# Kernel tuning notes

Measured on AMD Instinct MI355X. Metric: run time of the kernel, lower is better.

The kernel has to match this reference:

```python
import jax, jax.numpy as jnp
import numpy as np

B, L, PRED = 32, 1024, 256
CIN = 32            # enc_in == dec_in == c_out
DM, DFF, H, M = 512, 2048, 8, 64
E = DM // H
EL, DL = 2, 1
K = 25              # moving-avg kernel


def moving_avg(x):
    # torch: replicate-pad (K-1)//2 on both ends, then AvgPool1d(K, stride=1)
    pad = (K - 1) // 2
    xp = jnp.concatenate([jnp.repeat(x[:, :1], pad, axis=1), x, jnp.repeat(x[:, -1:], pad, axis=1)], axis=1)
    cs = jnp.cumsum(xp, axis=1)
    cs = jnp.concatenate([jnp.zeros_like(cs[:, :1]), cs], axis=1)
    return (cs[:, K:] - cs[:, :-K]) / K


def decomp(x):
    ma = moving_avg(x)
    return x - ma, ma


def circ_conv3(x, W):
    # Conv1d(kernel=3, padding=1, padding_mode='circular', bias=False); x:[B,L,C], W:[O,C,3]
    xp = jnp.concatenate([x[:, -1:], x, x[:, :1]], axis=1)
    win = jnp.stack([xp[:, :-2], xp[:, 1:-1], xp[:, 2:]], axis=-1)  # [B,L,C,3]
    return jnp.einsum('blcj,ocj->blo', win, W)


def pos_emb():
    pos = jnp.arange(L, dtype=jnp.float32)[:, None]
    div = jnp.exp(jnp.arange(0, DM, 2, dtype=jnp.float32) * (-np.log(10000.0) / DM))
    pe = jnp.zeros((L, DM), dtype=jnp.float32)
    pe = pe.at[:, 0::2].set(jnp.sin(pos * div))
    pe = pe.at[:, 1::2].set(jnp.cos(pos * div))
    return pe


def fourier_self(q, k, v, w):
    # FourierBlock: rFFT over time, keep lowest M modes, per-(head,mode) complex matmul, irFFT
    Bq, Lq = q.shape[0], q.shape[1]
    xft = jnp.fft.rfft(q.transpose(0, 2, 3, 1), axis=-1)[..., :M]        # [B,H,E,M]
    wc = w[..., 0] + 1j * w[..., 1]                                      # [H,E,E,M]
    om = jnp.einsum('bhem,heom->bhom', xft, wc)
    out_ft = jnp.zeros((Bq, H, E, Lq // 2 + 1), dtype=om.dtype).at[..., :M].set(om)
    return jnp.fft.irfft(out_ft, n=Lq, axis=-1).transpose(0, 3, 1, 2)    # [B,L,H,E]


def fourier_cross(q, k, v, w):
    # FourierCrossAttention (activation='tanh'); note official code uses k-modes as values
    Bq, Lq = q.shape[0], q.shape[1]
    xq = jnp.fft.rfft(q.transpose(0, 2, 3, 1), axis=-1)[..., :M]         # [B,H,E,M]
    xk = jnp.fft.rfft(k.transpose(0, 2, 3, 1), axis=-1)[..., :M]
    qk = jnp.tanh(jnp.einsum('bhex,bhey->bhxy', xq, xk))                 # complex tanh
    qkv = jnp.einsum('bhxy,bhey->bhex', qk, xk)
    wc = w[..., 0] + 1j * w[..., 1]
    om = jnp.einsum('bhex,heox->bhox', qkv, wc)
    out_ft = jnp.zeros((Bq, H, E, Lq // 2 + 1), dtype=om.dtype).at[..., :M].set(om)
    return jnp.fft.irfft(out_ft / (DM * DM), n=Lq, axis=-1).transpose(0, 3, 1, 2)


def mha(xq, xkv, Wq, bq, Wk, bk, Wv, bv, Wo, bo, inner, fw):
    Bq, Lq = xq.shape[0], xq.shape[1]
    q = (xq @ Wq.T + bq).reshape(Bq, Lq, H, E)
    k = (xkv @ Wk.T + bk).reshape(Bq, -1, H, E)
    v = (xkv @ Wv.T + bv).reshape(Bq, -1, H, E)
    o = inner(q, k, v, fw).reshape(Bq, Lq, DM)
    return o @ Wo.T + bo


def setup_inputs():
    ks = iter(jax.random.split(jax.random.key(0), 80))
    p = lambda shape: jax.random.normal(next(ks), shape, dtype=jnp.float32) * 0.02
    z = lambda shape: jnp.zeros(shape, dtype=jnp.float32)
    d = {}
    d['x_enc'] = jax.random.normal(next(ks), (B, L, CIN), dtype=jnp.float32)
    d['tok_W'] = p((DM, CIN, 3))
    for pre, n in (('enc_', EL), ('dec_s', DL), ('dec_c', DL)):
        for nm in ('Wq', 'Wk', 'Wv', 'Wo'):
            d[pre + nm] = p((n, DM, DM))
        for nm in ('bq', 'bk', 'bv', 'bo'):
            d[pre + nm] = z((n, DM))
    d['enc_c1W'] = p((EL, DFF, DM)); d['enc_c1b'] = z((EL, DFF))
    d['enc_c2W'] = p((EL, DM, DFF)); d['enc_c2b'] = z((EL, DM))
    d['dec_c1W'] = p((DL, DFF, DM)); d['dec_c1b'] = z((DL, DFF))
    d['dec_c2W'] = p((DL, DM, DFF)); d['dec_c2b'] = z((DL, DM))
    d['dec_trW'] = p((DL, CIN, DM, 3))
    d['fb_enc'] = p((H, E, E, M, 2))
    d['fb_dec'] = p((H, E, E, M, 2))
    d['fc_w'] = p((H, E, E, M, 2))
    d['p1W'] = p((CIN, CIN)); d['p1b'] = z((CIN,))
    d['p2W'] = p((PRED, L)); d['p2b'] = z((PRED,))
    d['p3W'] = p((CIN, DM)); d['p3b'] = z((CIN,))
    return d


def reference(x_enc, tok_W, enc_Wq, enc_Wk, enc_Wv, enc_Wo, enc_bq, enc_bk, enc_bv, enc_bo,
              dec_sWq, dec_sWk, dec_sWv, dec_sWo, dec_sbq, dec_sbk, dec_sbv, dec_sbo,
              dec_cWq, dec_cWk, dec_cWv, dec_cWo, dec_cbq, dec_cbk, dec_cbv, dec_cbo,
              enc_c1W, enc_c1b, enc_c2W, enc_c2b, dec_c1W, dec_c1b, dec_c2W, dec_c2b,
              dec_trW, fb_enc, fb_dec, fc_w, p1W, p1b, p2W, p2b, p3W, p3b):
    seasonal_init, trend_init = decomp(x_enc)
    enc = circ_conv3(x_enc, tok_W) + pos_emb()[None]   # DataEmbedding (eval: no dropout)
    for l in range(EL):
        h = enc + mha(enc, enc, enc_Wq[l], enc_bq[l], enc_Wk[l], enc_bk[l], enc_Wv[l], enc_bv[l],
                      enc_Wo[l], enc_bo[l], fourier_self, fb_enc)
        h, _ = decomp(h)
        y = jax.nn.relu(h @ enc_c1W[l].T + enc_c1b[l]) @ enc_c2W[l].T + enc_c2b[l]
        enc, _ = decomp(h + y)
    # NB: top-level source calls decoder(enc_out, enc_out, ...): dec_embedding output is unused
    x = enc
    trend = trend_init
    for l in range(DL):
        x = x + mha(x, x, dec_sWq[l], dec_sbq[l], dec_sWk[l], dec_sbk[l], dec_sWv[l], dec_sbv[l],
                    dec_sWo[l], dec_sbo[l], fourier_self, fb_dec)
        x, t1 = decomp(x)
        x = x + mha(x, enc, dec_cWq[l], dec_cbq[l], dec_cWk[l], dec_cbk[l], dec_cWv[l], dec_cbv[l],
                    dec_cWo[l], dec_cbo[l], fourier_cross, fc_w)
        x, t2 = decomp(x)
        y = jax.nn.relu(x @ dec_c1W[l].T + dec_c1b[l]) @ dec_c2W[l].T + dec_c2b[l]
        x, t3 = decomp(x + y)
        trend = trend + circ_conv3(t1 + t2 + t3, dec_trW[l])   # trend projection (circular conv3)
    out = trend + (x @ p3W.T + p3b)                            # [B,L,CIN]
    out = out @ p1W.T + p1b
    out = jnp.einsum('blc,pl->bpc', out, p2W) + p2b[None, :, None]  # proj2 over time -> [B,PRED,CIN]
    return out
```

## Files before the change

kernel.cpp:

```cpp
#include <hip/hip_runtime.h>
#include <math.h>

namespace {

constexpr int cB = 32, cL = 1024, cCIN = 32, cDM = 512, cDFF = 2048;
constexpr int cH = 8, cE = 64, cM = 64, cPRED = 256;
constexpr int M2 = 2 * cM;

typedef __attribute__((ext_vector_type(8))) short short8v;
typedef __attribute__((ext_vector_type(4))) float float4v;

__device__ inline unsigned short f2bf(float f) {
  unsigned int u = __builtin_bit_cast(unsigned int, f);
  u += 0x7FFFu + ((u >> 16) & 1u);
  return (unsigned short)(u >> 16);
}
__device__ inline float bf2f(unsigned short s) {
  return __builtin_bit_cast(float, (unsigned int)s << 16);
}

typedef const __attribute__((address_space(1))) unsigned int gu32_t;
typedef __attribute__((address_space(3))) unsigned int lu32_t;
__device__ inline void gld16(const void* g, void* l) {
  __builtin_amdgcn_global_load_lds((gu32_t*)g, (lu32_t*)l, 16, 0, 0);
}

__global__ void basis_kernel(short* __restrict__ basisdb, short* __restrict__ basisib) {
  int idx = blockIdx.x * 256 + threadIdx.x;
  if (idx >= M2 * cL) return;
  int t = idx & (cL - 1);
  int m2 = idx >> 10;
  int m = m2 >> 1;
  float ang = 6.2831853071795864f * (float)((m * t) & (cL - 1)) / (float)cL;
  float cv = cosf(ang), sv = sinf(ang);
  float vd = (m2 & 1) ? -sv : cv;
  basisdb[idx] = (short)f2bf(vd);
  float s = (m == 0) ? ((m2 & 1) ? 0.f : (1.f / (float)cL)) : (2.f / (float)cL);
  basisib[t * M2 + m2] = (short)f2bf(vd * s);
}

__global__ void pe_kernel(float* __restrict__ pe) {
  int idx = blockIdx.x * 256 + threadIdx.x;
  int o = idx & (cDM - 1), t = idx >> 9;
  int i = o >> 1;
  float freq = __expf((float)(2 * i) * (-9.210340371976184f / (float)cDM));
  float ang = freq * (float)t;
  pe[idx] = (o & 1) ? cosf(ang) : sinf(ang);
}

constexpr int NJOB = 14;
struct CvtArgs {
  const float* src[NJOB];
  short* dst[NJOB];
  int n[NJOB];
};
__global__ void cvtm_kernel(CvtArgs a) {
  int j = blockIdx.y;
  const float* s = a.src[j];
  short* d = a.dst[j];
  int n = a.n[j];
  for (int i = blockIdx.x * 256 + threadIdx.x; i < n; i += gridDim.x * 256)
    d[i] = (short)f2bf(s[i]);
}

__global__ void prep_kernel(const float* __restrict__ tok_W, const float* __restrict__ trW,
                            const float* __restrict__ p3W, const float* __restrict__ p3b,
                            short* __restrict__ Bpadb, short* __restrict__ Wtr3b,
                            short* __restrict__ p3padb, float* __restrict__ p3bpadf) {
  int idx = blockIdx.x * 256 + threadIdx.x;
  if (idx < 512 * 128) {
    int o = idx >> 7, s = idx & 127, j = s >> 5, c = s & 31;
    Bpadb[idx] = (j < 3) ? (short)f2bf(tok_W[o * 96 + c * 3 + j]) : (short)0;
  }
  if (idx < 128 * 1536) {
    int o = idx / 1536, r = idx % 1536, j = r >> 9, c = r & 511;
    Wtr3b[idx] = (o < 32) ? (short)f2bf(trW[(long)o * 1536 + c * 3 + j]) : (short)0;
  }
  if (idx < 128 * 512) {
    int o = idx >> 9, k = idx & 511;
    p3padb[idx] = (o < 32) ? (short)f2bf(p3W[o * 512 + k]) : (short)0;
  }
  if (idx < 128) p3bpadf[idx] = (idx < 32) ? p3b[idx] : 0.f;
}

__global__ void winbuild_kernel(const float* __restrict__ x, short* __restrict__ win) {
  int idx = blockIdx.x * 256 + threadIdx.x;
  int s4 = idx & 31;
  int row = idx >> 5;
  int t = row & (cL - 1), b = row >> 10;
  int j = s4 >> 3, c4 = s4 & 7;
  unsigned int lo = 0, hi = 0;
  if (j < 3) {
    int ts = (t + j + cL - 1) & (cL - 1);
    float4 v = *(const float4*)&x[((long)b * cL + ts) * cCIN + c4 * 4];
    lo = (unsigned int)f2bf(v.x) | ((unsigned int)f2bf(v.y) << 16);
    hi = (unsigned int)f2bf(v.z) | ((unsigned int)f2bf(v.w) << 16);
  }
  *(uint2*)&win[row * 128 + s4 * 4] = make_uint2(lo, hi);
}

__global__ __launch_bounds__(256) void transpose_bf(const short* __restrict__ in,
                                                    short* __restrict__ out) {
  __shared__ short tile[32][33];
  int b = blockIdx.z;
  in += (long)b * cL * cDM;
  out += (long)b * cL * cDM;
  int c0 = blockIdx.x * 32, t0 = blockIdx.y * 32;
  int tx = threadIdx.x & 31, ty = threadIdx.x >> 5;
#pragma unroll
  for (int r = 0; r < 32; r += 8) tile[ty + r][tx] = in[(long)(t0 + ty + r) * cDM + c0 + tx];
  __syncthreads();
#pragma unroll
  for (int r = 0; r < 32; r += 8)
    out[(long)(c0 + ty + r) * cL + t0 + tx] = tile[tx][ty + r];
}

__global__ void decomp_kernel(const float* __restrict__ x, float* __restrict__ maf, int n8,
                              int C) {
  int idx = blockIdx.x * 256 + threadIdx.x;
  if (idx >= n8) return;
  int c = idx % C;
  int u = idx / C;
  int t0 = (u & 127) * 8;
  int b = u >> 7;
  long base = (long)b * cL * C + c;
  float s = 0.f;
#pragma unroll
  for (int j = -12; j <= 12; j++) {
    int tt = t0 + j;
    tt = tt < 0 ? 0 : (tt >= cL ? cL - 1 : tt);
    s += x[base + (long)tt * C];
  }
#pragma unroll
  for (int k = 0; k < 8; k++) {
    int t = t0 + k;
    maf[base + (long)t * C] = s * (1.0f / 25.0f);
    int ta = t + 13;
    ta = ta >= cL ? cL - 1 : ta;
    int td = t - 12;
    td = td < 0 ? 0 : td;
    s += x[base + (long)ta * C] - x[base + (long)td * C];
  }
}

__global__ void decompb_kernel(const short* __restrict__ x, short* __restrict__ sb,
                               short* __restrict__ mab, int maacc, int n8, int C) {
  int idx = blockIdx.x * 256 + threadIdx.x;
  if (idx >= n8) return;
  int c = idx % C;
  int u = idx / C;
  int t0 = (u & 127) * 8;
  int b = u >> 7;
  long base = (long)b * cL * C + c;
  float s = 0.f;
#pragma unroll
  for (int j = -12; j <= 12; j++) {
    int tt = t0 + j;
    tt = tt < 0 ? 0 : (tt >= cL ? cL - 1 : tt);
    s += bf2f((unsigned short)x[base + (long)tt * C]);
  }
#pragma unroll
  for (int k = 0; k < 8; k++) {
    int t = t0 + k;
    long e = base + (long)t * C;
    float ma = s * (1.0f / 25.0f);
    if (sb) sb[e] = (short)f2bf(bf2f((unsigned short)x[e]) - ma);
    if (mab) {
      float v = maacc ? bf2f((unsigned short)mab[e]) + ma : ma;
      mab[e] = (short)f2bf(v);
    }
    int ta = t + 13;
    ta = ta >= cL ? cL - 1 : ta;
    int td = t - 12;
    td = td < 0 ? 0 : td;
    s += bf2f((unsigned short)x[base + (long)ta * C]) - bf2f((unsigned short)x[base + (long)td * C]);
  }
}

__global__ __launch_bounds__(256) void p2_kernel(const float* __restrict__ x,
                                                 const float* __restrict__ W,
                                                 const float* __restrict__ bias,
                                                 float* __restrict__ out) {
  __shared__ float tile[256 * 32];
  int b = blockIdx.x;
  int p0 = blockIdx.y * 8;
  int c = threadIdx.x & 31, pl = threadIdx.x >> 5;
  const float* xb = x + (long)b * cL * cCIN;
  const float* w = W + (long)(p0 + pl) * cL;
  float s = 0.f;
  for (int l0 = 0; l0 < cL; l0 += 256) {
    __syncthreads();
    for (int i = threadIdx.x; i < 256 * 32; i += 256) tile[i] = xb[(long)l0 * 32 + i];
    __syncthreads();
#pragma unroll 8
    for (int l = 0; l < 256; l++) s += tile[l * 32 + c] * w[l0 + l];
  }
  out[((long)b * cPRED + p0 + pl) * cCIN + c] = s + bias[p0 + pl];
}

__global__ __launch_bounds__(512) void modemix_t_kernel(const float* __restrict__ F,
                                                        const unsigned short* __restrict__ W,
                                                        short* __restrict__ Gt, float scale) {
  int b = blockIdx.x, h = blockIdx.y;
  __shared__ float2 Fs[cE][cM];
  __shared__ short ot[128][72];
  const float* Fb = F + ((long)b * cDM + h * cE) * M2;
  for (int i = threadIdx.x; i < cE * cM; i += 512) {
    int e = i >> 6, x = i & 63;
    Fs[e][x] = ((const float2*)(Fb + (long)e * M2))[x];
  }
  __syncthreads();
  int x = threadIdx.x & 63, og = threadIdx.x >> 6;
  float2 acc[8];
#pragma unroll
  for (int i = 0; i < 8; i++) acc[i] = make_float2(0.f, 0.f);
  for (int e = 0; e < cE; e++) {
    float2 f = Fs[e][x];
#pragma unroll
    for (int i = 0; i < 8; i++) {
      int o = og * 8 + i;
      unsigned int wu = *(const unsigned int*)&W[((((long)h * cE + e) * cE + o) * cM + x) * 2];
      float wx = bf2f((unsigned short)wu), wy = bf2f((unsigned short)(wu >> 16));
      acc[i].x += f.x * wx - f.y * wy;
      acc[i].y += f.x * wy + f.y * wx;
    }
  }
#pragma unroll
  for (int i = 0; i < 8; i++) {
    int o = og * 8 + i;
    ot[2 * x][o] = (short)f2bf(acc[i].x * scale);
    ot[2 * x + 1][o] = (short)f2bf(acc[i].y * scale);
  }
  __syncthreads();
  short* gb = Gt + (long)b * (M2 * cDM) + h * cE;
  for (int u = threadIdx.x; u < 1024; u += 512) {
    int row = u >> 3, seg = u & 7;
    *(uint4*)&gb[(long)row * cDM + seg * 8] = *(const uint4*)&ot[row][seg * 8];
  }
}

__global__ __launch_bounds__(1024) void fused_cross_kernel(const float* __restrict__ Fq,
                                                           const float* __restrict__ Fk,
                                                           const unsigned short* __restrict__ W,
                                                           short* __restrict__ Gt, float scale) {
  __shared__ __align__(16) char smem[65536];
  float2(*KsT)[cE] = (float2(*)[cE])smem;
  float2(*qks)[cM] = (float2(*)[cM])(smem + 32768);
  int b = blockIdx.x, h = blockIdx.y;
  const float* kb = Fk + ((long)b * cDM + h * cE) * M2;
  for (int i = threadIdx.x; i < cE * cM; i += 1024) {
    int e = i >> 6, y = i & 63;
    KsT[y][e] = ((const float2*)(kb + (long)e * M2))[y];
  }
  __syncthreads();
  {
    int x = threadIdx.x & 63, yg = threadIdx.x >> 6;
    const float* qb = Fq + ((long)b * cDM + h * cE) * M2;
    float2 acc[4];
#pragma unroll
    for (int i = 0; i < 4; i++) acc[i] = make_float2(0.f, 0.f);
    for (int e = 0; e < cE; e++) {
      float2 q = ((const float2*)(qb + (long)e * M2))[x];
#pragma unroll
      for (int i = 0; i < 4; i++) {
        float2 k = KsT[yg * 4 + i][e];
        acc[i].x += q.x * k.x - q.y * k.y;
        acc[i].y += q.x * k.y + q.y * k.x;
      }
    }
#pragma unroll
    for (int i = 0; i < 4; i++) {
      int y = yg * 4 + i;
      float a = acc[i].x, bi = acc[i].y;
      float re, im;
      float t2a = 2.f * a;
      if (fabsf(t2a) > 60.f) {
        re = t2a > 0.f ? 1.f : -1.f;
        im = 0.f;
      } else {
        float denom = coshf(t2a) + cosf(2.f * bi);
        re = sinhf(t2a) / denom;
        im = sinf(2.f * bi) / denom;
      }
      qks[y][x] = make_float2(re, im);
    }
  }
  __syncthreads();
  int e = threadIdx.x & 63, xg = threadIdx.x >> 6;
  float2 a2[4];
#pragma unroll
  for (int i = 0; i < 4; i++) a2[i] = make_float2(0.f, 0.f);
  for (int y = 0; y < cM; y++) {
    float2 k = KsT[y][e];
#pragma unroll
    for (int i = 0; i < 4; i++) {
      float2 qk = qks[y][xg * 4 + i];
      a2[i].x += qk.x * k.x - qk.y * k.y;
      a2[i].y += qk.x * k.y + qk.y * k.x;
    }
  }
  __syncthreads();
  float2(*Qv)[cM] = (float2(*)[cM])smem;
#pragma unroll
  for (int i = 0; i < 4; i++) Qv[e][xg * 4 + i] = a2[i];
  __syncthreads();
  {
    int x = threadIdx.x & 63, og = threadIdx.x >> 6;
    float2 m[4];
#pragma unroll
    for (int i = 0; i < 4; i++) m[i] = make_float2(0.f, 0.f);
    for (int ee = 0; ee < cE; ee++) {
      float2 f = Qv[ee][x];
#pragma unroll
      for (int i = 0; i < 4; i++) {
        int o = og * 4 + i;
        unsigned int wu = *(const unsigned int*)&W[((((long)h * cE + ee) * cE + o) * cM + x) * 2];
        float wx = bf2f((unsigned short)wu), wy = bf2f((unsigned short)(wu >> 16));
        m[i].x += f.x * wx - f.y * wy;
        m[i].y += f.x * wy + f.y * wx;
      }
    }
    short(*ot)[72] = (short(*)[72])(smem + 32768);
#pragma unroll
    for (int i = 0; i < 4; i++) {
      int o = og * 4 + i;
      ot[2 * x][o] = (short)f2bf(m[i].x * scale);
      ot[2 * x + 1][o] = (short)f2bf(m[i].y * scale);
    }
    __syncthreads();
    short* gb = Gt + (long)b * (M2 * cDM) + h * cE;
    int u = threadIdx.x;
    {
      int row = u >> 3, seg = u & 7;
      *(uint4*)&gb[(long)row * cDM + seg * 8] =
          *(const uint4*)&((short(*)[72])(smem + 32768))[row][seg * 8];
    }
  }
}

constexpr int GBM = 128, GBN = 128, GBK = 16, LPAD = 132;

__global__ __launch_bounds__(256) void gemm_kernel(const float* __restrict__ A,
                                                   const float* __restrict__ B,
                                                   const float* __restrict__ bias,
                                                   float* __restrict__ C, int M, int N, int K) {
  __shared__ float As[GBK][LPAD];
  __shared__ float Bs[GBK][LPAD];
  int n0 = blockIdx.x * GBN, m0 = blockIdx.y * GBM;
  int tid = threadIdx.x;
  int tx = tid & 15, ty = tid >> 4;
  float acc[8][8];
#pragma unroll
  for (int i = 0; i < 8; i++)
#pragma unroll
    for (int j = 0; j < 8; j++) acc[i][j] = 0.f;

  for (int k0 = 0; k0 < K; k0 += GBK) {
#pragma unroll
    for (int p = 0; p < 8; p++) {
      int i = p * 256 + tid;
      int mm = i >> 4, kk = i & 15;
      int gm = m0 + mm;
      As[kk][mm] = (gm < M && k0 + kk < K) ? A[(long)gm * K + k0 + kk] : 0.f;
    }
#pragma unroll
    for (int p = 0; p < 8; p++) {
      int i = p * 256 + tid;
      int nn = i >> 4, kk = i & 15;
      int gn = n0 + nn;
      Bs[kk][nn] = (gn < N && k0 + kk < K) ? B[(long)gn * K + k0 + kk] : 0.f;
    }
    __syncthreads();
#pragma unroll
    for (int kk = 0; kk < GBK; kk++) {
      float a[8], bb[8];
      *(float4*)&a[0] = *(const float4*)&As[kk][ty * 8];
      *(float4*)&a[4] = *(const float4*)&As[kk][ty * 8 + 4];
      *(float4*)&bb[0] = *(const float4*)&Bs[kk][tx * 8];
      *(float4*)&bb[4] = *(const float4*)&Bs[kk][tx * 8 + 4];
#pragma unroll
      for (int i = 0; i < 8; i++)
#pragma unroll
        for (int j = 0; j < 8; j++) acc[i][j] += a[i] * bb[j];
    }
    __syncthreads();
  }

  for (int i = 0; i < 8; i++) {
    int gm = m0 + ty * 8 + i;
    if (gm >= M) break;
    long rowoff = (long)gm * N;
    for (int j = 0; j < 8; j++) {
      int gn = n0 + tx * 8 + j;
      if (gn < N) C[rowoff + gn] = acc[i][j] + (bias ? bias[gn] : 0.f);
    }
  }
}

__global__ __launch_bounds__(512) void mfma_gemm256(
    const short* __restrict__ A, const short* __restrict__ B, const float* __restrict__ bias,
    const short* __restrict__ addendb, const float* __restrict__ pe, float* __restrict__ Cf,
    short* __restrict__ Cb, int M, int N, int K, int lda, int relu, int ldc) {
  __shared__ __align__(16) short As[16384];
  __shared__ __align__(16) short Bs[8192];
  int nwg = gridDim.x * gridDim.y;
  int orig = blockIdx.x + gridDim.x * blockIdx.y;
  int q = nwg >> 3, r = nwg & 7;
  int xcd = orig & 7, ii = orig >> 3;
  int flat = (xcd < r ? xcd * (q + 1) : r * (q + 1) + (xcd - r) * q) + ii;
  int bx = flat % (int)gridDim.x;
  int by = flat / (int)gridDim.x;

  int n0 = bx * 128, m0 = by * 256;
  int tid = threadIdx.x;
  int lane = tid & 63;
  int w = tid >> 6;
  int wm = w >> 1;
  int wn = w & 1;
  int lr = lane & 15, lg = lane >> 4;
  int lrow = lane >> 3;
  int scol = ((lane & 7) * 8) ^ (lrow << 3);

  float4v acc[4][4];
#pragma unroll
  for (int i = 0; i < 4; i++)
#pragma unroll
    for (int j = 0; j < 4; j++) acc[i][j] = (float4v){0.f, 0.f, 0.f, 0.f};

  int nk = K >> 6;
  int swr = (lr & 7) << 3;
  for (int t = 0; t < nk; ++t) {
    int k0 = t << 6;
#pragma unroll
    for (int j = 0; j < 4; j++) {
      int seg = w * 4 + j;
      int row = seg * 8 + lrow;
      gld16(A + (long)(m0 + row) * lda + k0 + scol, &As[seg * 512]);
    }
#pragma unroll
    for (int j = 0; j < 2; j++) {
      int seg = w * 2 + j;
      int row = seg * 8 + lrow;
      gld16(B + (long)(n0 + row) * K + k0 + scol, &Bs[seg * 512]);
    }
    asm volatile("s_waitcnt vmcnt(0)" ::: "memory");
    __syncthreads();
#pragma unroll
    for (int ks = 0; ks < 2; ks++) {
      short8v af[4], bfr[4];
#pragma unroll
      for (int mi = 0; mi < 4; mi++)
        af[mi] = *(const short8v*)&As[(wm * 64 + mi * 16 + lr) * 64 + ((ks * 32 + lg * 8) ^ swr)];
#pragma unroll
      for (int ni = 0; ni < 4; ni++)
        bfr[ni] = *(const short8v*)&Bs[(wn * 64 + ni * 16 + lr) * 64 + ((ks * 32 + lg * 8) ^ swr)];
#pragma unroll
      for (int mi = 0; mi < 4; mi++)
#pragma unroll
        for (int ni = 0; ni < 4; ni++)
          acc[mi][ni] =
              __builtin_amdgcn_mfma_f32_16x16x32_bf16(af[mi], bfr[ni], acc[mi][ni], 0, 0, 0);
    }
    __syncthreads();
  }

#pragma unroll
  for (int mi = 0; mi < 4; mi++) {
#pragma unroll
    for (int i = 0; i < 4; i++) {
      int gr = m0 + wm * 64 + mi * 16 + lg * 4 + i;
      long rowoff = (long)gr * ldc;
#pragma unroll
      for (int ni = 0; ni < 4; ni++) {
        int gc = n0 + wn * 64 + ni * 16 + lr;
        float v = acc[mi][ni][i];
        if (bias) v += bias[gc];
        if (pe) v += pe[((gr & (cL - 1)) << 9) + gc];
        if (addendb) v += bf2f((unsigned short)addendb[rowoff + gc]);
        if (relu) v = fmaxf(v, 0.f);
        if (Cf) Cf[rowoff + gc] = v;
        if (Cb) Cb[rowoff + gc] = (short)f2bf(v);
      }
    }
  }
}

__global__ __launch_bounds__(256) void mfma_gemm64(
    const short* __restrict__ A, const short* __restrict__ B, const float* __restrict__ bias,
    const float* __restrict__ addf, const short* __restrict__ addb,
    const float* __restrict__ m0b, float* __restrict__ Cf, short* __restrict__ Cb, int M, int N,
    int K, int lda, long sA, long sB, long sC, int Nreal, int ldc, int amode,
    const short* __restrict__ A2, const short* __restrict__ B2, const float* __restrict__ m0b2,
    float* __restrict__ Cf2, int zsplit) {
  __shared__ __align__(16) short As[4096];
  __shared__ __align__(16) short Bs[4096];
  int nwg = gridDim.x * gridDim.y * gridDim.z;
  int orig = blockIdx.x + gridDim.x * (blockIdx.y + gridDim.y * blockIdx.z);
  int q = nwg >> 3, r = nwg & 7;
  int xcd = orig & 7, ii = orig >> 3;
  int flat = (xcd < r ? xcd * (q + 1) : r * (q + 1) + (xcd - r) * q) + ii;
  int bx = flat % (int)gridDim.x;
  int tmp = flat / (int)gridDim.x;
  int by = tmp % (int)gridDim.y;
  int bz = tmp / (int)gridDim.y;

  int z = bz;
  if (zsplit > 0 && bz >= zsplit) {
    A = A2;
    B = B2;
    m0b = m0b2;
    Cf = Cf2;
    z = bz - zsplit;
  }
  A += (long)z * sA;
  B += (long)z * sB;
  if (Cf) Cf += (long)z * sC;
  if (Cb) Cb += (long)z * sC;
  const float* Ad = addf ? addf + (long)z * sC : nullptr;
  const short* Adb = addb ? addb + (long)z * sC : nullptr;
  int n0 = bx * 64, m0 = by * 64;
  int tid = threadIdx.x;
  int lane = tid & 63;
  int w = tid >> 6;
  int wm = w & 1, wn = w >> 1;
  int lr = lane & 15, lg = lane >> 4;
  int lrow = lane >> 3;
  int scol = ((lane & 7) * 8) ^ (lrow << 3);

  float4v acc[2][2];
#pragma unroll
  for (int i = 0; i < 2; i++)
#pragma unroll
    for (int j = 0; j < 2; j++) acc[i][j] = (float4v){0.f, 0.f, 0.f, 0.f};

  int nk = K >> 6;
  int swr = (lr & 7) << 3;
  for (int t = 0; t < nk; ++t) {
    int k0 = t << 6;
#pragma unroll
    for (int j = 0; j < 2; j++) {
      int seg = w * 2 + j;
      int row = seg * 8 + lrow;
      const short* ga;
      if (amode == 0) {
        ga = A + (long)(m0 + row) * lda + k0 + scol;
      } else {
        int r2 = m0 + row;
        int bb = r2 >> 10, tt = r2 & 1023;
        int jj = k0 >> 9, c0 = k0 & 511;
        ga = A + ((((long)(bb << 10)) | ((tt + jj + 1023) & 1023)) << 9) + c0 + scol;
      }
      gld16(ga, &As[seg * 512]);
      gld16(B + (long)(n0 + row) * K + k0 + scol, &Bs[seg * 512]);
    }
    asm volatile("s_waitcnt vmcnt(0)" ::: "memory");
    __syncthreads();
#pragma unroll
    for (int ks = 0; ks < 2; ks++) {
      short8v af[2], bfr[2];
#pragma unroll
      for (int mi = 0; mi < 2; mi++)
        af[mi] = *(const short8v*)&As[(wm * 32 + mi * 16 + lr) * 64 + ((ks * 32 + lg * 8) ^ swr)];
#pragma unroll
      for (int ni = 0; ni < 2; ni++)
        bfr[ni] = *(const short8v*)&Bs[(wn * 32 + ni * 16 + lr) * 64 + ((ks * 32 + lg * 8) ^ swr)];
#pragma unroll
      for (int mi = 0; mi < 2; mi++)
#pragma unroll
        for (int ni = 0; ni < 2; ni++)
          acc[mi][ni] =
              __builtin_amdgcn_mfma_f32_16x16x32_bf16(af[mi], bfr[ni], acc[mi][ni], 0, 0, 0);
    }
    __syncthreads();
  }

#pragma unroll
  for (int mi = 0; mi < 2; mi++) {
#pragma unroll
    for (int i = 0; i < 4; i++) {
      int gr = m0 + wm * 32 + mi * 16 + lg * 4 + i;
      long rowoff = (long)gr * ldc;
#pragma unroll
      for (int ni = 0; ni < 2; ni++) {
        int gc = n0 + wn * 32 + ni * 16 + lr;
        if (gc < Nreal) {
          float v = acc[mi][ni][i];
          if (bias) v += bias[gc];
          if (m0b && gc == 0) v += 1024.f * m0b[gr];
          if (Ad) v += Ad[rowoff + gc];
          if (Adb) v += bf2f((unsigned short)Adb[rowoff + gc]);
          if (Cf) Cf[rowoff + gc] = v;
          if (Cb) Cb[rowoff + gc] = (short)f2bf(v);
        }
      }
    }
  }
}

}

extern "C" void kernel_launch(void* const* d_in, const int* in_sizes, int n_in, void* d_out,
                              int out_size, void* d_ws, size_t ws_size, hipStream_t stream) {
  const float* x_enc = (const float*)d_in[0];
  const float* tok_W = (const float*)d_in[1];
  const float* enc_Wq = (const float*)d_in[2];
  const float* enc_Wo = (const float*)d_in[5];
  const float* enc_bq = (const float*)d_in[6];
  const float* enc_bo = (const float*)d_in[9];
  const float* dsWq = (const float*)d_in[10];
  const float* dsWo = (const float*)d_in[13];
  const float* dsbq = (const float*)d_in[14];
  const float* dsbo = (const float*)d_in[17];
  const float* dcWq = (const float*)d_in[18];
  const float* dcWk = (const float*)d_in[19];
  const float* dcWo = (const float*)d_in[21];
  const float* dcbq = (const float*)d_in[22];
  const float* dcbk = (const float*)d_in[23];
  const float* dcbo = (const float*)d_in[25];
  const float* enc_c1W = (const float*)d_in[26];
  const float* enc_c1b = (const float*)d_in[27];
  const float* enc_c2W = (const float*)d_in[28];
  const float* enc_c2b = (const float*)d_in[29];
  const float* dec_c1W = (const float*)d_in[30];
  const float* dec_c1b = (const float*)d_in[31];
  const float* dec_c2W = (const float*)d_in[32];
  const float* dec_c2b = (const float*)d_in[33];
  const float* dec_trW = (const float*)d_in[34];
  const float* fb_enc = (const float*)d_in[35];
  const float* fb_dec = (const float*)d_in[36];
  const float* fc_w = (const float*)d_in[37];
  const float* p1W = (const float*)d_in[38];
  const float* p1b = (const float*)d_in[39];
  const float* p2W = (const float*)d_in[40];
  const float* p2b = (const float*)d_in[41];
  const float* p3W = (const float*)d_in[42];
  const float* p3b = (const float*)d_in[43];

  constexpr long MIXW = 8L * 64 * 64 * 64 * 2;

  auto layout_bytes = [&](long BG, long RH) -> size_t {
    size_t t = 0;
    auto add = [&](size_t b) { t = (t + b + 255) & ~(size_t)255; };
    add(2 * 262144 * 2); add(2 * 262144 * 2);
    add(262144 * 2); add(262144 * 2); add(262144 * 2); add(262144 * 2); add(262144 * 2);
    add(2 * 1048576 * 2); add(2 * 1048576 * 2); add(1048576 * 2); add(1048576 * 2);
    add(131072 * 2); add(131072 * 2); add(65536 * 2); add(196608 * 2); add(65536 * 2);
    add(128 * 4); add(524288 * 4);
    add(MIXW * 2); add(MIXW * 2); add(MIXW * 2);
    long GA = BG * cL * cDM;
    add(GA * 2); add(GA * 2); add(GA * 2); add(GA * 2); add(GA * 2);
    add(BG * cL * 128 * 2);
    size_t ub = (size_t)GA * 2;
    size_t hd = (size_t)RH * cDFF * 2;
    add(ub > hd ? ub : hd);
    add(BG * 65536 * 4); add(BG * 65536 * 4);
    add(BG * 65536 * 2); add(BG * 65536 * 2); add(BG * 65536 * 2); add(BG * 65536 * 2);
    add(BG * cL * cCIN * 4); add(BG * cL * cCIN * 4); add(BG * cL * cCIN * 4);
    return t;
  };
  int BG = cB;
  while (BG > 1 && layout_bytes(BG, 512) > ws_size) BG >>= 1;
  long RH = (long)BG * cL;
  while (RH > 512 && layout_bytes(BG, RH) > ws_size) RH >>= 1;

  long GBL = (long)BG * cL;
  char* base = (char*)d_ws;
  size_t off = 0;
  auto alloc = [&](size_t bytes) -> void* {
    void* p = base + off;
    off = (off + bytes + 255) & ~(size_t)255;
    return p;
  };
  short* WqbE = (short*)alloc(2 * 262144 * 2);
  short* WobE = (short*)alloc(2 * 262144 * 2);
  short* dsWqb = (short*)alloc(262144 * 2);
  short* dsWob = (short*)alloc(262144 * 2);
  short* dcWqb = (short*)alloc(262144 * 2);
  short* dcWkb = (short*)alloc(262144 * 2);
  short* dcWob = (short*)alloc(262144 * 2);
  short* c1bE = (short*)alloc(2 * 1048576 * 2);
  short* c2bE = (short*)alloc(2 * 1048576 * 2);
  short* c1bD = (short*)alloc(1048576 * 2);
  short* c2bD = (short*)alloc(1048576 * 2);
  short* basisdb = (short*)alloc(131072 * 2);
  short* basisib = (short*)alloc(131072 * 2);
  short* Bpadb = (short*)alloc(65536 * 2);
  short* Wtr3b = (short*)alloc(196608 * 2);
  short* p3padb = (short*)alloc(65536 * 2);
  float* p3bpadf = (float*)alloc(128 * 4);
  float* pe = (float*)alloc(524288 * 4);
  short* fbEb = (short*)alloc(MIXW * 2);
  short* fbDb = (short*)alloc(MIXW * 2);
  short* fcwb = (short*)alloc(MIXW * 2);
  long GA = GBL * cDM;
  short* Eb = (short*)alloc(GA * 2);
  short* Xb = (short*)alloc(GA * 2);
  short* Ab = (short*)alloc(GA * 2);
  short* Sb = (short*)alloc(GA * 2);
  short* Yb = (short*)alloc(GA * 2);
  short* winb = (short*)alloc(GBL * 128 * 2);
  size_t ubsz = (size_t)GA * 2;
  size_t hdsz = (size_t)RH * cDFF * 2;
  short* UB = (short*)alloc(ubsz > hdsz ? ubsz : hdsz);
  short* Tb = UB;
  short* HDb = UB;
  float* Fq = (float*)alloc((size_t)BG * 65536 * 4);
  float* Fk = (float*)alloc((size_t)BG * 65536 * 4);
  short* FEb = (short*)alloc((size_t)BG * 65536 * 2);
  short* FXb = (short*)alloc((size_t)BG * 65536 * 2);
  short* Gtb = (short*)alloc((size_t)BG * 65536 * 2);
  short* Hb = (short*)alloc((size_t)BG * 65536 * 2);
  float* TRD = (float*)alloc(GBL * cCIN * 4);
  float* O1 = (float*)alloc(GBL * cCIN * 4);
  float* O2 = (float*)alloc(GBL * cCIN * 4);

  auto mg256 = [&](const short* Am, const short* Bm, const float* bias, const short* adb,
                   const float* peA, float* Cf, short* Cb, int Mm, int Nn, int Kk, int lda,
                   int relu, int ldc) {
    dim3 g(Nn / 128, Mm / 256);
    mfma_gemm256<<<g, 512, 0, stream>>>(Am, Bm, bias, adb, peA, Cf, Cb, Mm, Nn, Kk, lda, relu,
                                        ldc);
  };
  auto mg64 = [&](const short* Am, const short* Bm, const float* bias, const float* addf,
                  const short* addb, const float* m0b, float* Cf, short* Cb, int Mm, int Nn,
                  int Kk, int lda, long sA, long sB, long sC, int batch, int Nreal, int ldc,
                  int amode) {
    dim3 g(Nn / 64, Mm / 64, batch);
    mfma_gemm64<<<g, 256, 0, stream>>>(Am, Bm, bias, addf, addb, m0b, Cf, Cb, Mm, Nn, Kk, lda,
                                       sA, sB, sC, Nreal, ldc, amode, nullptr, nullptr, nullptr,
                                       nullptr, 0);
  };
  auto decompf = [&](const float* x, float* maf, long total, int C_) {
    int n8 = (int)(total / 8);
    decomp_kernel<<<(n8 + 255) / 256, 256, 0, stream>>>(x, maf, n8, C_);
  };
  auto decompb = [&](const short* x, short* sb, short* mab, int maacc, long total, int C_) {
    int n8 = (int)(total / 8);
    decompb_kernel<<<(n8 + 255) / 256, 256, 0, stream>>>(x, sb, mab, maacc, n8, C_);
  };
  auto dft = [&](const short* srcb, short* Fout) {
    transpose_bf<<<dim3(16, 32, BG), 256, 0, stream>>>(srcb, Tb);
    mg64(basisdb, Tb, nullptr, nullptr, nullptr, nullptr, nullptr, Fout, M2, cDM, cL, cL, 0,
         (long)cDM * cL, 65536, BG, cDM, cDM, 0);
  };
  auto modeproj = [&](const short* Wb, const short* Fin, const float* m0b, float* Cf, short* Cb) {
    mg64(Wb, Fin, nullptr, nullptr, nullptr, m0b, Cf, Cb, cDM, M2, cDM, cDM, 0, 65536, 65536, BG,
         M2, M2, 0);
  };
  auto modeproj2 = [&](const short* Wa, const short* Fa, const float* ba, float* Ca,
                       const short* Wb2, const short* Fb2, const float* bb2, float* Cb2) {
    dim3 g(M2 / 64, cDM / 64, 2 * BG);
    mfma_gemm64<<<g, 256, 0, stream>>>(Wa, Fa, nullptr, nullptr, nullptr, ba, Ca, nullptr, cDM,
                                       M2, cDM, cDM, 0, 65536, 65536, M2, M2, 0, Wb2, Fb2, bb2,
                                       Cb2, BG);
  };
  auto idft = [&](const short* Hin, const float* bias, const short* adb, short* Cbout) {
    mg64(basisib, Hin, bias, nullptr, adb, nullptr, nullptr, Cbout, cL, cDM, M2, M2, 0, 65536,
         (long)cL * cDM, BG, cDM, cDM, 0);
  };
  auto ffn = [&](const short* inb, const short* addb, short* outb, const short* c1w,
                 const float* c1bias, const short* c2w, const float* c2bias) {
    for (long r = 0; r < GBL; r += RH) {
      mg256(inb + r * cDM, c1w, c1bias, nullptr, nullptr, nullptr, HDb, (int)RH, cDFF, cDM, cDM,
            1, cDFF);
      mg256(HDb, c2w, c2bias, addb + r * cDM, nullptr, nullptr, outb + r * cDM, (int)RH, cDM,
            cDFF, cDFF, 0, cDM);
    }
  };
  auto trendg = [&](const short* mab) {
    mg64(mab, Wtr3b, nullptr, TRD, nullptr, nullptr, TRD, nullptr, (int)GBL, 64, 1536, 512, 0, 0,
         0, 1, cCIN, cCIN, 1);
  };
  auto mixt = [&](const float* F, const short* W, float scale) {
    modemix_t_kernel<<<dim3(BG, cH), 512, 0, stream>>>(F, (const unsigned short*)W, Gtb, scale);
  };

  basis_kernel<<<(M2 * cL) / 256, 256, 0, stream>>>(basisdb, basisib);
  pe_kernel<<<(cL * cDM) / 256, 256, 0, stream>>>(pe);
  prep_kernel<<<768, 256, 0, stream>>>(tok_W, dec_trW, p3W, p3b, Bpadb, Wtr3b, p3padb, p3bpadf);
  {
    CvtArgs ca;
    const float* srcs[NJOB] = {enc_Wq, enc_Wo, dsWq, dsWo, dcWq, dcWk, dcWo,
                               enc_c1W, enc_c2W, dec_c1W, dec_c2W, fb_enc, fb_dec, fc_w};
    short* dsts[NJOB] = {WqbE, WobE, dsWqb, dsWob, dcWqb, dcWkb, dcWob,
                         c1bE, c2bE, c1bD, c2bD, fbEb, fbDb, fcwb};
    int ns[NJOB] = {524288, 524288, 262144, 262144, 262144, 262144, 262144,
                    2097152, 2097152, 1048576, 1048576, (int)MIXW, (int)MIXW, (int)MIXW};
    for (int j = 0; j < NJOB; j++) {
      ca.src[j] = srcs[j];
      ca.dst[j] = dsts[j];
      ca.n[j] = ns[j];
    }
    cvtm_kernel<<<dim3(256, NJOB), 256, 0, stream>>>(ca);
  }

  for (int b0 = 0; b0 < cB; b0 += BG) {
    const float* xg = x_enc + (long)b0 * cL * cCIN;

    decompf(xg, TRD, GBL * cCIN, cCIN);
    winbuild_kernel<<<(int)(GBL * 32 / 256), 256, 0, stream>>>(xg, winb);
    mg256(winb, Bpadb, nullptr, nullptr, pe, nullptr, Eb, (int)GBL, cDM, 128, 128, 0, cDM);

    for (int l = 0; l < 2; l++) {
      dft(Eb, FEb);
      modeproj(WqbE + (long)l * 262144, FEb, enc_bq + l * cDM, Fq, nullptr);
      mixt(Fq, fbEb, 1.0f);
      modeproj(WobE + (long)l * 262144, Gtb, nullptr, nullptr, Hb);
      idft(Hb, enc_bo + l * cDM, Eb, Yb);
      decompb(Yb, Xb, nullptr, 0, GA, cDM);
      ffn(Xb, Xb, Yb, c1bE + (long)l * 1048576, enc_c1b + l * cDFF, c2bE + (long)l * 1048576,
          enc_c2b + l * cDM);
      decompb(Yb, Eb, nullptr, 0, GA, cDM);
    }

    dft(Eb, FEb);
    modeproj(dsWqb, FEb, dsbq, Fq, nullptr);
    mixt(Fq, fbDb, 1.0f);
    modeproj(dsWob, Gtb, nullptr, nullptr, Hb);
    idft(Hb, dsbo, Eb, Yb);
    decompb(Yb, Xb, Sb, 0, GA, cDM);
    dft(Xb, FXb);
    modeproj2(dcWqb, FXb, dcbq, Fq, dcWkb, FEb, dcbk, Fk);
    fused_cross_kernel<<<dim3(BG, cH), 1024, 0, stream>>>(Fq, Fk, (const unsigned short*)fcwb,
                                                          Gtb, 1.0f / (float)(cDM * cDM));
    modeproj(dcWob, Gtb, nullptr, nullptr, Hb);
    idft(Hb, dcbo, Xb, Yb);
    decompb(Yb, Ab, Sb, 1, GA, cDM);
    ffn(Ab, Ab, Yb, c1bD, dec_c1b, c2bD, dec_c2b);
    decompb(Yb, Xb, Sb, 1, GA, cDM);
    trendg(Sb);

    mg64(Xb, p3padb, p3bpadf, TRD, nullptr, nullptr, O1, nullptr, (int)GBL, 64, cDM, cDM, 0, 0,
         0, 1, cCIN, cCIN, 0);
    gemm_kernel<<<dim3(1, (int)(GBL / 128)), 256, 0, stream>>>(O1, p1W, p1b, O2, (int)GBL, cCIN,
                                                               cCIN);
    p2_kernel<<<dim3(BG, 32), 256, 0, stream>>>(O2, p2W, p2b,
                                                (float*)d_out + (long)b0 * cPRED * cCIN);
  }
}
```

Baseline: 2.101 ms.

## Fuse query mode projection with Fourier mode mixing; widen transpose tiles

```diff
diff --git a/kernel.cpp b/kernel.cpp
--- a/kernel.cpp
+++ b/kernel.cpp
@@ -101,17 +101,17 @@
 
 __global__ __launch_bounds__(256) void transpose_bf(const short* __restrict__ in,
                                                     short* __restrict__ out) {
-  __shared__ short tile[32][33];
+  __shared__ short tile[64][65];
   int b = blockIdx.z;
   in += (long)b * cL * cDM;
   out += (long)b * cL * cDM;
-  int c0 = blockIdx.x * 32, t0 = blockIdx.y * 32;
-  int tx = threadIdx.x & 31, ty = threadIdx.x >> 5;
-#pragma unroll
-  for (int r = 0; r < 32; r += 8) tile[ty + r][tx] = in[(long)(t0 + ty + r) * cDM + c0 + tx];
+  int c0 = blockIdx.x * 64, t0 = blockIdx.y * 64;
+  int tx = threadIdx.x & 63, ty = threadIdx.x >> 6;
+#pragma unroll
+  for (int r = 0; r < 64; r += 4) tile[ty + r][tx] = in[(long)(t0 + ty + r) * cDM + c0 + tx];
   __syncthreads();
 #pragma unroll
-  for (int r = 0; r < 32; r += 8)
+  for (int r = 0; r < 64; r += 4)
     out[(long)(c0 + ty + r) * cL + t0 + tx] = tile[tx][ty + r];
 }
 
@@ -198,42 +198,108 @@
   out[((long)b * cPRED + p0 + pl) * cCIN + c] = s + bias[p0 + pl];
 }
 
-__global__ __launch_bounds__(512) void modemix_t_kernel(const float* __restrict__ F,
-                                                        const unsigned short* __restrict__ W,
-                                                        short* __restrict__ Gt, float scale) {
+__global__ __launch_bounds__(256) void projmix_kernel(const short* __restrict__ W,
+                                                      const short* __restrict__ Fin,
+                                                      const float* __restrict__ bias,
+                                                      const unsigned short* __restrict__ Wm,
+                                                      short* __restrict__ Gt, float scale) {
+  __shared__ __align__(16) char smem[51968];
+  short* As = (short*)smem;
+  short* Bs = (short*)(smem + 8192);
   int b = blockIdx.x, h = blockIdx.y;
-  __shared__ float2 Fs[cE][cM];
-  __shared__ short ot[128][72];
-  const float* Fb = F + ((long)b * cDM + h * cE) * M2;
-  for (int i = threadIdx.x; i < cE * cM; i += 512) {
-    int e = i >> 6, x = i & 63;
-    Fs[e][x] = ((const float2*)(Fb + (long)e * M2))[x];
+  const short* Wa = W + (long)(h * 64) * 512;
+  const short* Fb = Fin + (long)b * 65536;
+  int tid = threadIdx.x;
+  int lane = tid & 63;
+  int w = tid >> 6;
+  int lr = lane & 15, lg = lane >> 4;
+  int lrow = lane >> 3;
+  int scol = ((lane & 7) * 8) ^ (lrow << 3);
+  int swr = (lr & 7) << 3;
+
+  float4v acc[4][2];
+#pragma unroll
+  for (int i = 0; i < 4; i++)
+#pragma unroll
+    for (int j = 0; j < 2; j++) acc[i][j] = (float4v){0.f, 0.f, 0.f, 0.f};
+
+  for (int t = 0; t < 8; ++t) {
+    int k0 = t << 6;
+#pragma unroll
+    for (int j = 0; j < 2; j++) {
+      int seg = w * 2 + j;
+      int row = seg * 8 + lrow;
+      gld16(Wa + (long)row * 512 + k0 + scol, &As[seg * 512]);
+    }
+#pragma unroll
+    for (int j = 0; j < 4; j++) {
+      int seg = w * 4 + j;
+      int row = seg * 8 + lrow;
+      gld16(Fb + (long)row * 512 + k0 + scol, &Bs[seg * 512]);
+    }
+    asm volatile("s_waitcnt vmcnt(0)" ::: "memory");
+    __syncthreads();
+#pragma unroll
+    for (int ks = 0; ks < 2; ks++) {
+      short8v af[4], bfr[2];
+#pragma unroll
+      for (int mi = 0; mi < 4; mi++)
+        af[mi] = *(const short8v*)&As[(mi * 16 + lr) * 64 + ((ks * 32 + lg * 8) ^ swr)];
+#pragma unroll
+      for (int ni = 0; ni < 2; ni++)
+        bfr[ni] = *(const short8v*)&Bs[(w * 32 + ni * 16 + lr) * 64 + ((ks * 32 + lg * 8) ^ swr)];
+#pragma unroll
+      for (int mi = 0; mi < 4; mi++)
+#pragma unroll
+        for (int ni = 0; ni < 2; ni++)
+          acc[mi][ni] =
+              __builtin_amdgcn_mfma_f32_16x16x32_bf16(af[mi], bfr[ni], acc[mi][ni], 0, 0, 0);
+    }
+    __syncthreads();
+  }
+
+  float* Fsf = (float*)smem;
+  short(*ot)[72] = (short(*)[72])(smem + 33280);
+#pragma unroll
+  for (int mi = 0; mi < 4; mi++) {
+#pragma unroll
+    for (int i = 0; i < 4; i++) {
+      int gr = mi * 16 + lg * 4 + i;
+#pragma unroll
+      for (int ni = 0; ni < 2; ni++) {
+        int gc = w * 32 + ni * 16 + lr;
+        float v = acc[mi][ni][i];
+        if (gc == 0 && bias) v += 1024.f * bias[h * 64 + gr];
+        Fsf[gr * 130 + gc] = v;
+      }
+    }
   }
   __syncthreads();
-  int x = threadIdx.x & 63, og = threadIdx.x >> 6;
-  float2 acc[8];
-#pragma unroll
-  for (int i = 0; i < 8; i++) acc[i] = make_float2(0.f, 0.f);
+
+  int x = tid & 63, og = tid >> 6;
+  float2 m[16];
+#pragma unroll
+  for (int i = 0; i < 16; i++) m[i] = make_float2(0.f, 0.f);
   for (int e = 0; e < cE; e++) {
-    float2 f = Fs[e][x];
-#pragma unroll
-    for (int i = 0; i < 8; i++) {
-      int o = og * 8 + i;
-      unsigned int wu = *(const unsigned int*)&W[((((long)h * cE + e) * cE + o) * cM + x) * 2];
+    float2 f = *(const float2*)&Fsf[e * 130 + 2 * x];
+#pragma unroll
+    for (int i = 0; i < 16; i++) {
+      int o = og * 16 + i;
+      unsigned int wu = *(const unsigned int*)&Wm[((((long)h * cE + e) * cE + o) * cM + x) * 2];
       float wx = bf2f((unsigned short)wu), wy = bf2f((unsigned short)(wu >> 16));
-      acc[i].x += f.x * wx - f.y * wy;
-      acc[i].y += f.x * wy + f.y * wx;
-    }
-  }
-#pragma unroll
-  for (int i = 0; i < 8; i++) {
-    int o = og * 8 + i;
-    ot[2 * x][o] = (short)f2bf(acc[i].x * scale);
-    ot[2 * x + 1][o] = (short)f2bf(acc[i].y * scale);
+      m[i].x += f.x * wx - f.y * wy;
+      m[i].y += f.x * wy + f.y * wx;
+    }
+  }
+#pragma unroll
+  for (int i = 0; i < 16; i++) {
+    int o = og * 16 + i;
+    ot[2 * x][o] = (short)f2bf(m[i].x * scale);
+    ot[2 * x + 1][o] = (short)f2bf(m[i].y * scale);
   }
   __syncthreads();
   short* gb = Gt + (long)b * (M2 * cDM) + h * cE;
-  for (int u = threadIdx.x; u < 1024; u += 512) {
+  for (int u = tid; u < 1024; u += 256) {
     int row = u >> 3, seg = u & 7;
     *(uint4*)&gb[(long)row * cDM + seg * 8] = *(const uint4*)&ot[row][seg * 8];
   }
@@ -739,9 +805,13 @@
     decompb_kernel<<<(n8 + 255) / 256, 256, 0, stream>>>(x, sb, mab, maacc, n8, C_);
   };
   auto dft = [&](const short* srcb, short* Fout) {
-    transpose_bf<<<dim3(16, 32, BG), 256, 0, stream>>>(srcb, Tb);
+    transpose_bf<<<dim3(8, 16, BG), 256, 0, stream>>>(srcb, Tb);
     mg64(basisdb, Tb, nullptr, nullptr, nullptr, nullptr, nullptr, Fout, M2, cDM, cL, cL, 0,
          (long)cDM * cL, 65536, BG, cDM, cDM, 0);
+  };
+  auto projmix = [&](const short* Wq, const short* Fin, const float* bq, const short* Wmix) {
+    projmix_kernel<<<dim3(BG, cH), 256, 0, stream>>>(Wq, Fin, bq, (const unsigned short*)Wmix,
+                                                     Gtb, 1.0f);
   };
   auto modeproj = [&](const short* Wb, const short* Fin, const float* m0b, float* Cf, short* Cb) {
     mg64(Wb, Fin, nullptr, nullptr, nullptr, m0b, Cf, Cb, cDM, M2, cDM, cDM, 0, 65536, 65536, BG,
@@ -770,9 +840,6 @@
   auto trendg = [&](const short* mab) {
     mg64(mab, Wtr3b, nullptr, TRD, nullptr, nullptr, TRD, nullptr, (int)GBL, 64, 1536, 512, 0, 0,
          0, 1, cCIN, cCIN, 1);
-  };
-  auto mixt = [&](const float* F, const short* W, float scale) {
-    modemix_t_kernel<<<dim3(BG, cH), 512, 0, stream>>>(F, (const unsigned short*)W, Gtb, scale);
   };
 
   basis_kernel<<<(M2 * cL) / 256, 256, 0, stream>>>(basisdb, basisib);
@@ -803,8 +870,7 @@
 
     for (int l = 0; l < 2; l++) {
       dft(Eb, FEb);
-      modeproj(WqbE + (long)l * 262144, FEb, enc_bq + l * cDM, Fq, nullptr);
-      mixt(Fq, fbEb, 1.0f);
+      projmix(WqbE + (long)l * 262144, FEb, enc_bq + l * cDM, fbEb);
       modeproj(WobE + (long)l * 262144, Gtb, nullptr, nullptr, Hb);
       idft(Hb, enc_bo + l * cDM, Eb, Yb);
       decompb(Yb, Xb, nullptr, 0, GA, cDM);
@@ -814,8 +880,7 @@
     }
 
     dft(Eb, FEb);
-    modeproj(dsWqb, FEb, dsbq, Fq, nullptr);
-    mixt(Fq, fbDb, 1.0f);
+    projmix(dsWqb, FEb, dsbq, fbDb);
     modeproj(dsWob, Gtb, nullptr, nullptr, Hb);
     idft(Hb, dsbo, Eb, Yb);
     decompb(Yb, Xb, Sb, 0, GA, cDM);
```

After: 2.079 ms. Within noise of the previous version (-1.1%).
